# Kernel optimization log

Hardware: AMD Instinct MI355X
Metric: run time of the kernel (lower is better)

## Reference

```python
import jax, jax.numpy as jnp
import numpy as np

N_USER = 50000
N_ITEM = 100000
N = N_USER + N_ITEM
D = 64
NNZ = 2_400_000
B = 4096
N_LAYERS = 3
NEG_SLOPE = 0.01  # F.leaky_relu default
EPS = 1e-12       # F.normalize default eps


def setup_inputs() -> dict:
    key = jax.random.key(0)
    ks = jax.random.split(key, 12)
    s = 0.1  # xavier-ish scale
    return {
        "user_emb": jax.random.normal(ks[0], (N_USER, D), jnp.float32) * s,
        "item_emb": jax.random.normal(ks[1], (N_ITEM, D), jnp.float32) * s,
        "W_gc": jax.random.normal(ks[2], (N_LAYERS, D, D), jnp.float32) * s,
        "W_bi": jax.random.normal(ks[3], (N_LAYERS, D, D), jnp.float32) * s,
        "b_bi": jax.random.normal(ks[4], (N_LAYERS, 1, D), jnp.float32) * s,
        "vals": jax.random.uniform(ks[5], (NNZ,), jnp.float32) * (1.0 / 16.0),
        "rows": jax.random.randint(ks[6], (NNZ,), 0, N, jnp.int32),
        "cols": jax.random.randint(ks[7], (NNZ,), 0, N, jnp.int32),
        "users": jax.random.randint(ks[8], (B,), 0, N_USER, jnp.int32),
        "pos_items": jax.random.randint(ks[9], (B,), 0, N_ITEM, jnp.int32),
        "neg_items": jax.random.randint(ks[10], (B,), 0, N_ITEM, jnp.int32),
    }


def _spmm(rows, cols, vals, E, n):
    # sparse [n,n] (COO) @ dense [n,d]
    return jax.ops.segment_sum(vals[:, None] * E[cols], rows, num_segments=n)


def reference(user_emb, item_emb, W_gc, W_bi, b_bi, vals, rows, cols,
              users, pos_items, neg_items):
    n_user = user_emb.shape[0]
    n = n_user + item_emb.shape[0]
    ego = jnp.concatenate([user_emb, item_emb], axis=0)  # [N, D]
    all_embs = [ego]
    for k in range(N_LAYERS):
        L_side = _spmm(rows, cols, vals, ego, n)        # L @ E
        LI_side = L_side + ego                           # (L + I) @ E
        # NOTE: original code adds b_bi to BOTH branches (b_gc unused)
        sum_e = LI_side @ W_gc[k] + b_bi[k]
        bi_e = (L_side * ego) @ W_bi[k] + b_bi[k]
        ego = jax.nn.leaky_relu(sum_e + bi_e, NEG_SLOPE)
        norm = ego / jnp.maximum(
            jnp.linalg.norm(ego, axis=1, keepdims=True), EPS)
        all_embs.append(norm)
    all_embs = jnp.concatenate(all_embs, axis=1)         # [N, D*(L+1)]
    u_g = all_embs[:n_user][users]
    pos_g = all_embs[n_user:][pos_items]
    neg_g = all_embs[n_user:][neg_items]
    return (u_g, pos_g, neg_g)
```

## Files before the change

### kernel.cpp

```cpp
#include <hip/hip_runtime.h>

#define N_USER 50000
#define N_ITEM 100000
#define NTOT   150000
#define D      64
#define NNZ    2400000
#define NEG_SLOPE 0.01f

#define BSHIFT 10
#define NB     147
#define P1_PER 4096
#define NBLK1  586

typedef unsigned int uint;
typedef unsigned short ushort;
typedef _Float16 h4 __attribute__((ext_vector_type(4)));
typedef float f4 __attribute__((ext_vector_type(4)));

__device__ inline uint bf16rne(float x) {
    uint b = __float_as_uint(x);
    return (b + 0x7FFFu + ((b >> 16) & 1u)) >> 16;
}
__device__ inline float bf_lo(uint u) { return __uint_as_float(u << 16); }
__device__ inline float bf_hi(uint u) { return __uint_as_float(u & 0xFFFF0000u); }

__global__ void k_concat16(const float* __restrict__ u, const float* __restrict__ it,
                           ushort* __restrict__ A16) {
    int i = blockIdx.x * 256 + threadIdx.x;
    const int nu4 = N_USER * D / 4;
    float4 v = (i < nu4) ? ((const float4*)u)[i] : ((const float4*)it)[i - nu4];
    uint lo = bf16rne(v.x) | (bf16rne(v.y) << 16);
    uint hi = bf16rne(v.z) | (bf16rne(v.w) << 16);
    ((uint2*)A16)[i] = make_uint2(lo, hi);
}

__global__ void k_bzero(int* __restrict__ bcnt) {
    int t = threadIdx.x;
    if (t < NB) bcnt[t] = 0;
}

__global__ __launch_bounds__(1024) void k_bhist(const int* __restrict__ rows,
                                                int* __restrict__ bcnt) {
    __shared__ int lcnt[NB];
    int tid = threadIdx.x;
    if (tid < NB) lcnt[tid] = 0;
    __syncthreads();
    int base = blockIdx.x * P1_PER;
    #pragma unroll
    for (int k = 0; k < 4; ++k) {
        int i = base + k * 1024 + tid;
        if (i < NNZ) atomicAdd(&lcnt[rows[i] >> BSHIFT], 1);
    }
    __syncthreads();
    if (tid < NB) atomicAdd(&bcnt[tid], lcnt[tid]);
}

__global__ void k_bscan(const int* __restrict__ bcnt, int* __restrict__ bptr,
                        int* __restrict__ bcur) {
    __shared__ int s[256];
    int tid = threadIdx.x;
    int v = (tid < NB) ? bcnt[tid] : 0;
    s[tid] = v; __syncthreads();
    for (int off = 1; off < 256; off <<= 1) {
        int t = (tid >= off) ? s[tid - off] : 0;
        __syncthreads();
        s[tid] += t;
        __syncthreads();
    }
    if (tid < NB) { int ex = s[tid] - v; bptr[tid] = ex; bcur[tid] = ex; }
    if (tid == NB - 1) bptr[NB] = s[tid];
}

__global__ __launch_bounds__(1024) void k_binpass1(const int* __restrict__ rows,
                                                   const int* __restrict__ cols,
                                                   const float* __restrict__ vals,
                                                   int* __restrict__ bcur,
                                                   int2* __restrict__ bucketed) {
    __shared__ int lcnt[NB], lbase[NB];
    int tid = threadIdx.x;
    int base = blockIdx.x * P1_PER;
    if (tid < NB) lcnt[tid] = 0;
    __syncthreads();
    int r[4];
    #pragma unroll
    for (int k = 0; k < 4; ++k) {
        int i = base + k * 1024 + tid;
        r[k] = (i < NNZ) ? rows[i] : -1;
        if (r[k] >= 0) atomicAdd(&lcnt[r[k] >> BSHIFT], 1);
    }
    __syncthreads();
    if (tid < NB) { lbase[tid] = atomicAdd(&bcur[tid], lcnt[tid]); lcnt[tid] = 0; }
    __syncthreads();
    #pragma unroll
    for (int k = 0; k < 4; ++k) {
        int i = base + k * 1024 + tid;
        if (r[k] >= 0) {
            int b = r[k] >> BSHIFT;
            int off = atomicAdd(&lcnt[b], 1);
            bucketed[lbase[b] + off] =
                make_int2(((r[k] & 1023) << 18) | cols[i], __float_as_int(vals[i]));
        }
    }
}

__global__ __launch_bounds__(1024) void k_binpass2(const int* __restrict__ bptr,
                                                   const int2* __restrict__ bucketed,
                                                   int* __restrict__ ptr,
                                                   int2* __restrict__ csr) {
    __shared__ int c0[1024], px[1024];
    int tid = threadIdx.x, b = blockIdx.x;
    int s = bptr[b], e = bptr[b + 1];
    c0[tid] = 0;
    __syncthreads();
    for (int i = s + tid; i < e; i += 1024) atomicAdd(&c0[bucketed[i].x >> 18], 1);
    __syncthreads();
    int v = c0[tid];
    px[tid] = v;
    __syncthreads();
    for (int off = 1; off < 1024; off <<= 1) {
        int t = (tid >= off) ? px[tid - off] : 0;
        __syncthreads();
        px[tid] += t;
        __syncthreads();
    }
    int ex = px[tid] - v;
    int r = (b << BSHIFT) + tid;
    if (r <= NTOT) ptr[r] = s + ex;
    px[tid] = ex;
    c0[tid] = 0;
    __syncthreads();
    for (int i = s + tid; i < e; i += 1024) {
        int2 e2 = bucketed[i];
        int lr = e2.x >> 18;
        int off = atomicAdd(&c0[lr], 1);
        csr[s + px[lr] + off] = make_int2(e2.x & 0x3FFFF, e2.y);
    }
}

__global__ __launch_bounds__(256) void k_spmm(const int* __restrict__ ptr,
                                              const int2* __restrict__ csr,
                                              const ushort* __restrict__ E16,
                                              float* __restrict__ Lout) {
    int lane = threadIdx.x & 63;
    int half = lane >> 5;
    int l32  = lane & 31;
    int r = __builtin_amdgcn_readfirstlane(blockIdx.x * 4 + (threadIdx.x >> 6));
    int start = ptr[r], end = ptr[r + 1];
    float acc0 = 0.f, acc1 = 0.f;
    const uint* E32 = (const uint*)E16;
    int j = start;
    for (; j + 15 < end; j += 16) {
        int2 ea0 = csr[j + 0],  ea1 = csr[j + 1],  ea2 = csr[j + 2],  ea3 = csr[j + 3];
        int2 ea4 = csr[j + 4],  ea5 = csr[j + 5],  ea6 = csr[j + 6],  ea7 = csr[j + 7];
        int2 ea8 = csr[j + 8],  ea9 = csr[j + 9],  eaA = csr[j + 10], eaB = csr[j + 11];
        int2 eaC = csr[j + 12], eaD = csr[j + 13], eaE = csr[j + 14], eaF = csr[j + 15];
        int c0 = half ? ea1.x : ea0.x;
        int c1 = half ? ea3.x : ea2.x;
        int c2 = half ? ea5.x : ea4.x;
        int c3 = half ? ea7.x : ea6.x;
        int c4 = half ? ea9.x : ea8.x;
        int c5 = half ? eaB.x : eaA.x;
        int c6 = half ? eaD.x : eaC.x;
        int c7 = half ? eaF.x : eaE.x;
        uint u0 = E32[(c0 << 5) + l32];
        uint u1 = E32[(c1 << 5) + l32];
        uint u2 = E32[(c2 << 5) + l32];
        uint u3 = E32[(c3 << 5) + l32];
        uint u4 = E32[(c4 << 5) + l32];
        uint u5 = E32[(c5 << 5) + l32];
        uint u6 = E32[(c6 << 5) + l32];
        uint u7 = E32[(c7 << 5) + l32];
        float v0 = __int_as_float(half ? ea1.y : ea0.y);
        float v1 = __int_as_float(half ? ea3.y : ea2.y);
        float v2 = __int_as_float(half ? ea5.y : ea4.y);
        float v3 = __int_as_float(half ? ea7.y : ea6.y);
        float v4 = __int_as_float(half ? ea9.y : ea8.y);
        float v5 = __int_as_float(half ? eaB.y : eaA.y);
        float v6 = __int_as_float(half ? eaD.y : eaC.y);
        float v7 = __int_as_float(half ? eaF.y : eaE.y);
        acc0 += v0 * bf_lo(u0);  acc1 += v0 * bf_hi(u0);
        acc0 += v1 * bf_lo(u1);  acc1 += v1 * bf_hi(u1);
        acc0 += v2 * bf_lo(u2);  acc1 += v2 * bf_hi(u2);
        acc0 += v3 * bf_lo(u3);  acc1 += v3 * bf_hi(u3);
        acc0 += v4 * bf_lo(u4);  acc1 += v4 * bf_hi(u4);
        acc0 += v5 * bf_lo(u5);  acc1 += v5 * bf_hi(u5);
        acc0 += v6 * bf_lo(u6);  acc1 += v6 * bf_hi(u6);
        acc0 += v7 * bf_lo(u7);  acc1 += v7 * bf_hi(u7);
    }
    for (; j + 7 < end; j += 8) {
        int2 ea = csr[j + 0], eb = csr[j + 1];
        int2 ec = csr[j + 2], ed = csr[j + 3];
        int2 ee = csr[j + 4], ef = csr[j + 5];
        int2 eg = csr[j + 6], eh = csr[j + 7];
        int c0 = half ? eb.x : ea.x;
        int c1 = half ? ed.x : ec.x;
        int c2 = half ? ef.x : ee.x;
        int c3 = half ? eh.x : eg.x;
        uint u0 = E32[(c0 << 5) + l32];
        uint u1 = E32[(c1 << 5) + l32];
        uint u2 = E32[(c2 << 5) + l32];
        uint u3 = E32[(c3 << 5) + l32];
        float v0 = __int_as_float(half ? eb.y : ea.y);
        float v1 = __int_as_float(half ? ed.y : ec.y);
        float v2 = __int_as_float(half ? ef.y : ee.y);
        float v3 = __int_as_float(half ? eh.y : eg.y);
        acc0 += v0 * bf_lo(u0);  acc1 += v0 * bf_hi(u0);
        acc0 += v1 * bf_lo(u1);  acc1 += v1 * bf_hi(u1);
        acc0 += v2 * bf_lo(u2);  acc1 += v2 * bf_hi(u2);
        acc0 += v3 * bf_lo(u3);  acc1 += v3 * bf_hi(u3);
    }
    for (; j + 1 < end; j += 2) {
        int2 ea = csr[j], eb = csr[j + 1];
        int c   = half ? eb.x : ea.x;
        float v = __int_as_float(half ? eb.y : ea.y);
        uint u = E32[(c << 5) + l32];
        acc0 += v * bf_lo(u);  acc1 += v * bf_hi(u);
    }
    if (j < end) {
        int2 ea = csr[j];
        if (half == 0) {
            uint u = E32[(ea.x << 5) + l32];
            float v = __int_as_float(ea.y);
            acc0 += v * bf_lo(u);  acc1 += v * bf_hi(u);
        }
    }
    acc0 += __shfl_xor(acc0, 32, 64);
    acc1 += __shfl_xor(acc1, 32, 64);
    if (half == 0)
        *(float2*)&Lout[r * D + l32 * 2] = make_float2(acc0, acc1);
}

__global__ __launch_bounds__(256) void k_transform_mfma(
        const ushort* __restrict__ E16, const float* __restrict__ L,
        const float* __restrict__ Wgc, const float* __restrict__ Wbi,
        const float* __restrict__ bb, ushort* __restrict__ O16, int n) {
    __shared__ _Float16 ldsW[2 * 16 * 256];
    __shared__ ushort   ldsO[4][16 * 72];
    int tid = threadIdx.x;

    #pragma unroll
    for (int m = 0; m < 2; ++m) {
        const float* W = m ? Wbi : Wgc;
        for (int idx = tid; idx < 4096; idx += 256) {
            int k = idx >> 6, nn = idx & 63;
            ldsW[(m * 16 + (k >> 4) * 4 + (nn >> 4)) * 256 + (nn & 15) * 16 + (k & 15)] =
                (_Float16)W[idx];
        }
    }
    __syncthreads();

    int l = tid & 63, w = tid >> 6;
    int g = l >> 4, r16 = l & 15;

    h4 bfrag[2][4][4];
    #pragma unroll
    for (int m = 0; m < 2; ++m)
        #pragma unroll
        for (int ks = 0; ks < 4; ++ks)
            #pragma unroll
            for (int nt = 0; nt < 4; ++nt)
                bfrag[m][ks][nt] =
                    *(const h4*)&ldsW[(m * 16 + ks * 4 + nt) * 256 + r16 * 16 + g * 4];

    for (int t = 0; t < 4; ++t) {
        int tile = blockIdx.x * 4 + t;
        int rowbase = tile * 64 + w * 16;
        int r = rowbase + r16;
        int rc = min(r, n - 1);

        h4 x1[4], x2[4];
        #pragma unroll
        for (int ks = 0; ks < 4; ++ks) {
            int c = ks * 16 + g * 4;
            float4 lf = *(const float4*)&L[rc * D + c];
            uint2  eu = *(const uint2*)&E16[rc * D + c];
            float e0 = bf_lo(eu.x), e1 = bf_hi(eu.x);
            float e2 = bf_lo(eu.y), e3 = bf_hi(eu.y);
            x1[ks][0] = (_Float16)(lf.x + e0); x1[ks][1] = (_Float16)(lf.y + e1);
            x1[ks][2] = (_Float16)(lf.z + e2); x1[ks][3] = (_Float16)(lf.w + e3);
            x2[ks][0] = (_Float16)(lf.x * e0); x2[ks][1] = (_Float16)(lf.y * e1);
            x2[ks][2] = (_Float16)(lf.z * e2); x2[ks][3] = (_Float16)(lf.w * e3);
        }

        f4 acc[4];
        #pragma unroll
        for (int nt = 0; nt < 4; ++nt) acc[nt] = (f4){0.f, 0.f, 0.f, 0.f};
        #pragma unroll
        for (int ks = 0; ks < 4; ++ks)
            #pragma unroll
            for (int nt = 0; nt < 4; ++nt)
                acc[nt] = __builtin_amdgcn_mfma_f32_16x16x16f16(x1[ks], bfrag[0][ks][nt],
                                                                acc[nt], 0, 0, 0);
        #pragma unroll
        for (int ks = 0; ks < 4; ++ks)
            #pragma unroll
            for (int nt = 0; nt < 4; ++nt)
                acc[nt] = __builtin_amdgcn_mfma_f32_16x16x16f16(x2[ks], bfrag[1][ks][nt],
                                                                acc[nt], 0, 0, 0);

        #pragma unroll
        for (int nt = 0; nt < 4; ++nt) {
            int col = nt * 16 + r16;
            float bv = 2.f * bb[col];
            #pragma unroll
            for (int i = 0; i < 4; ++i) {
                float y = acc[nt][i] + bv;
                y = (y >= 0.f) ? y : NEG_SLOPE * y;
                ldsO[w][(g * 4 + i) * 72 + col] = (ushort)bf16rne(y);
            }
        }
        int lr = l >> 2;
        int rowg = rowbase + lr;
        if (rowg < n) {
            const ushort* src = &ldsO[w][lr * 72 + (l & 3) * 16];
            uint4 v0 = *(const uint4*)src;
            uint4 v1 = *(const uint4*)(src + 8);
            *(uint4*)&O16[rowg * D + (l & 3) * 16] = v0;
            *(uint4*)&O16[rowg * D + (l & 3) * 16 + 8] = v1;
        }
    }
}

__global__ void k_gather0(const float* __restrict__ u, const float* __restrict__ it,
                          const int* __restrict__ users, const int* __restrict__ pos,
                          const int* __restrict__ neg, float* __restrict__ out) {
    int lane = threadIdx.x & 63;
    int gi = blockIdx.x * 4 + (threadIdx.x >> 6);
    int g = gi >> 12, b = gi & 4095;
    const float* src = (g == 0) ? (u + (size_t)users[b] * D)
                                : (it + (size_t)((g == 1) ? pos[b] : neg[b]) * D);
    out[gi * 256 + lane] = src[lane];
}

__global__ void k_gathern(const ushort* __restrict__ E16, const int* __restrict__ users,
                          const int* __restrict__ pos, const int* __restrict__ neg,
                          float* __restrict__ out, int layer) {
    int lane = threadIdx.x & 63;
    int gi = blockIdx.x * 4 + (threadIdx.x >> 6);
    int g = gi >> 12, b = gi & 4095;
    int src = (g == 0) ? users[b] : (N_USER + ((g == 1) ? pos[b] : neg[b]));
    float v = __uint_as_float(((uint)E16[src * D + lane]) << 16);
    float ss = v * v;
    #pragma unroll
    for (int off = 32; off >= 1; off >>= 1) ss += __shfl_xor(ss, off, 64);
    float dnm = fmaxf(sqrtf(ss), 1e-12f);
    out[gi * 256 + layer * D + lane] = v / dnm;
}

extern "C" void kernel_launch(void* const* d_in, const int* in_sizes, int n_in,
                              void* d_out, int out_size, void* d_ws, size_t ws_size,
                              hipStream_t stream) {
    const float* user_emb = (const float*)d_in[0];
    const float* item_emb = (const float*)d_in[1];
    const float* W_gc     = (const float*)d_in[2];
    const float* W_bi     = (const float*)d_in[3];
    const float* b_bi     = (const float*)d_in[4];
    const float* vals     = (const float*)d_in[5];
    const int*   rows     = (const int*)d_in[6];
    const int*   cols     = (const int*)d_in[7];
    const int*   users    = (const int*)d_in[8];
    const int*   pos      = (const int*)d_in[9];
    const int*   neg      = (const int*)d_in[10];
    float* out = (float*)d_out;

    char* ws = (char*)d_ws;
    size_t off = 0;
    auto alloc = [&](size_t b) { void* p = ws + off; off += (b + 255) & ~(size_t)255; return p; };
    ushort* Ea  = (ushort*)alloc((size_t)NTOT * D * 2);
    ushort* Eb  = (ushort*)alloc((size_t)NTOT * D * 2);
    float*  L   = (float*) alloc((size_t)NTOT * D * 4);
    int2*   csr = (int2*)  alloc((size_t)NNZ * 8);
    int*    ptr = (int*)   alloc((size_t)(NTOT + 1) * 4);
    int*    bptr= (int*)   alloc((NB + 1) * 4);
    int*    bcnt= (int*)   alloc(NB * 4);
    int*    bcur= (int*)   alloc(NB * 4);
    int2*   bucketed = (int2*)L;
    (void)ws_size;

    hipLaunchKernelGGL(k_concat16, dim3(9375), dim3(256),  0, stream, user_emb, item_emb, Ea);
    hipLaunchKernelGGL(k_bzero,    dim3(1),    dim3(256),  0, stream, bcnt);
    hipLaunchKernelGGL(k_bhist,    dim3(NBLK1),dim3(1024), 0, stream, rows, bcnt);
    hipLaunchKernelGGL(k_bscan,    dim3(1),    dim3(256),  0, stream, bcnt, bptr, bcur);
    hipLaunchKernelGGL(k_binpass1, dim3(NBLK1),dim3(1024), 0, stream, rows, cols, vals, bcur, bucketed);
    hipLaunchKernelGGL(k_binpass2, dim3(NB),   dim3(1024), 0, stream, bptr, bucketed, ptr, csr);
    hipLaunchKernelGGL(k_gather0,  dim3(3072), dim3(256),  0, stream, user_emb, item_emb, users, pos, neg, out);

    ushort* cur = Ea; ushort* nxt = Eb;
    for (int k = 0; k < 3; ++k) {
        hipLaunchKernelGGL(k_spmm,           dim3(37500), dim3(256), 0, stream, ptr, csr, cur, L);
        hipLaunchKernelGGL(k_transform_mfma, dim3(586),   dim3(256), 0, stream, cur, L,
                           W_gc + k * 4096, W_bi + k * 4096, b_bi + k * 64, nxt, NTOT);
        hipLaunchKernelGGL(k_gathern,        dim3(3072),  dim3(256), 0, stream, nxt, users, pos, neg, out, k + 1);
        ushort* t = cur; cur = nxt; nxt = t;
    }
}
```

Baseline: 442.1 us.

## Fuse SpMM and MFMA transform into one per-layer kernel via LDS staging

Merges the sparse aggregation and the dense MFMA transform into a single kernel. Each wave computes 16 rows of L@E, forms the (L+E) and (L*E) operands in fp16 in LDS, and runs the MFMA directly. This removes the fp32 L intermediate write and re-read plus one launch per layer. In exchange each block repeats the weight staging, and each wave handles 16 rows serially, which lowers the parallelism available to hide gather latency. The bucketed scratch gets its own allocation.

```diff
diff --git a/kernel.cpp b/kernel.cpp
--- a/kernel.cpp
+++ b/kernel.cpp
@@ -11,6 +11,7 @@
 #define NB     147
 #define P1_PER 4096
 #define NBLK1  586
+#define NROWBLK 2344
 
 typedef unsigned int uint;
 typedef unsigned short ushort;
@@ -137,105 +138,14 @@
     }
 }
 
-__global__ __launch_bounds__(256) void k_spmm(const int* __restrict__ ptr,
-                                              const int2* __restrict__ csr,
-                                              const ushort* __restrict__ E16,
-                                              float* __restrict__ Lout) {
-    int lane = threadIdx.x & 63;
-    int half = lane >> 5;
-    int l32  = lane & 31;
-    int r = __builtin_amdgcn_readfirstlane(blockIdx.x * 4 + (threadIdx.x >> 6));
-    int start = ptr[r], end = ptr[r + 1];
-    float acc0 = 0.f, acc1 = 0.f;
-    const uint* E32 = (const uint*)E16;
-    int j = start;
-    for (; j + 15 < end; j += 16) {
-        int2 ea0 = csr[j + 0],  ea1 = csr[j + 1],  ea2 = csr[j + 2],  ea3 = csr[j + 3];
-        int2 ea4 = csr[j + 4],  ea5 = csr[j + 5],  ea6 = csr[j + 6],  ea7 = csr[j + 7];
-        int2 ea8 = csr[j + 8],  ea9 = csr[j + 9],  eaA = csr[j + 10], eaB = csr[j + 11];
-        int2 eaC = csr[j + 12], eaD = csr[j + 13], eaE = csr[j + 14], eaF = csr[j + 15];
-        int c0 = half ? ea1.x : ea0.x;
-        int c1 = half ? ea3.x : ea2.x;
-        int c2 = half ? ea5.x : ea4.x;
-        int c3 = half ? ea7.x : ea6.x;
-        int c4 = half ? ea9.x : ea8.x;
-        int c5 = half ? eaB.x : eaA.x;
-        int c6 = half ? eaD.x : eaC.x;
-        int c7 = half ? eaF.x : eaE.x;
-        uint u0 = E32[(c0 << 5) + l32];
-        uint u1 = E32[(c1 << 5) + l32];
-        uint u2 = E32[(c2 << 5) + l32];
-        uint u3 = E32[(c3 << 5) + l32];
-        uint u4 = E32[(c4 << 5) + l32];
-        uint u5 = E32[(c5 << 5) + l32];
-        uint u6 = E32[(c6 << 5) + l32];
-        uint u7 = E32[(c7 << 5) + l32];
-        float v0 = __int_as_float(half ? ea1.y : ea0.y);
-        float v1 = __int_as_float(half ? ea3.y : ea2.y);
-        float v2 = __int_as_float(half ? ea5.y : ea4.y);
-        float v3 = __int_as_float(half ? ea7.y : ea6.y);
-        float v4 = __int_as_float(half ? ea9.y : ea8.y);
-        float v5 = __int_as_float(half ? eaB.y : eaA.y);
-        float v6 = __int_as_float(half ? eaD.y : eaC.y);
-        float v7 = __int_as_float(half ? eaF.y : eaE.y);
-        acc0 += v0 * bf_lo(u0);  acc1 += v0 * bf_hi(u0);
-        acc0 += v1 * bf_lo(u1);  acc1 += v1 * bf_hi(u1);
-        acc0 += v2 * bf_lo(u2);  acc1 += v2 * bf_hi(u2);
-        acc0 += v3 * bf_lo(u3);  acc1 += v3 * bf_hi(u3);
-        acc0 += v4 * bf_lo(u4);  acc1 += v4 * bf_hi(u4);
-        acc0 += v5 * bf_lo(u5);  acc1 += v5 * bf_hi(u5);
-        acc0 += v6 * bf_lo(u6);  acc1 += v6 * bf_hi(u6);
-        acc0 += v7 * bf_lo(u7);  acc1 += v7 * bf_hi(u7);
-    }
-    for (; j + 7 < end; j += 8) {
-        int2 ea = csr[j + 0], eb = csr[j + 1];
-        int2 ec = csr[j + 2], ed = csr[j + 3];
-        int2 ee = csr[j + 4], ef = csr[j + 5];
-        int2 eg = csr[j + 6], eh = csr[j + 7];
-        int c0 = half ? eb.x : ea.x;
-        int c1 = half ? ed.x : ec.x;
-        int c2 = half ? ef.x : ee.x;
-        int c3 = half ? eh.x : eg.x;
-        uint u0 = E32[(c0 << 5) + l32];
-        uint u1 = E32[(c1 << 5) + l32];
-        uint u2 = E32[(c2 << 5) + l32];
-        uint u3 = E32[(c3 << 5) + l32];
-        float v0 = __int_as_float(half ? eb.y : ea.y);
-        float v1 = __int_as_float(half ? ed.y : ec.y);
-        float v2 = __int_as_float(half ? ef.y : ee.y);
-        float v3 = __int_as_float(half ? eh.y : eg.y);
-        acc0 += v0 * bf_lo(u0);  acc1 += v0 * bf_hi(u0);
-        acc0 += v1 * bf_lo(u1);  acc1 += v1 * bf_hi(u1);
-        acc0 += v2 * bf_lo(u2);  acc1 += v2 * bf_hi(u2);
-        acc0 += v3 * bf_lo(u3);  acc1 += v3 * bf_hi(u3);
-    }
-    for (; j + 1 < end; j += 2) {
-        int2 ea = csr[j], eb = csr[j + 1];
-        int c   = half ? eb.x : ea.x;
-        float v = __int_as_float(half ? eb.y : ea.y);
-        uint u = E32[(c << 5) + l32];
-        acc0 += v * bf_lo(u);  acc1 += v * bf_hi(u);
-    }
-    if (j < end) {
-        int2 ea = csr[j];
-        if (half == 0) {
-            uint u = E32[(ea.x << 5) + l32];
-            float v = __int_as_float(ea.y);
-            acc0 += v * bf_lo(u);  acc1 += v * bf_hi(u);
-        }
-    }
-    acc0 += __shfl_xor(acc0, 32, 64);
-    acc1 += __shfl_xor(acc1, 32, 64);
-    if (half == 0)
-        *(float2*)&Lout[r * D + l32 * 2] = make_float2(acc0, acc1);
-}
-
-__global__ __launch_bounds__(256) void k_transform_mfma(
-        const ushort* __restrict__ E16, const float* __restrict__ L,
+#define XPITCH 136
+__global__ __launch_bounds__(256) void k_layer(
+        const int* __restrict__ ptr, const int2* __restrict__ csr,
+        const ushort* __restrict__ E16,
         const float* __restrict__ Wgc, const float* __restrict__ Wbi,
-        const float* __restrict__ bb, ushort* __restrict__ O16, int n) {
+        const float* __restrict__ bb, ushort* __restrict__ O16) {
     __shared__ _Float16 ldsW[2 * 16 * 256];
-    __shared__ ushort   ldsO[4][16 * 72];
+    __shared__ ushort   xbuf[4][16 * XPITCH];
     int tid = threadIdx.x;
 
     #pragma unroll
@@ -249,8 +159,11 @@
     }
     __syncthreads();
 
-    int l = tid & 63, w = tid >> 6;
-    int g = l >> 4, r16 = l & 15;
+    int lane = tid & 63, w = tid >> 6;
+    int half = lane >> 5, l32 = lane & 31;
+    int g = lane >> 4, r16 = lane & 15;
+    const uint* E32 = (const uint*)E16;
+    _Float16* xw = (_Float16*)&xbuf[w][0];
 
     h4 bfrag[2][4][4];
     #pragma unroll
@@ -262,62 +175,142 @@
                 bfrag[m][ks][nt] =
                     *(const h4*)&ldsW[(m * 16 + ks * 4 + nt) * 256 + r16 * 16 + g * 4];
 
-    for (int t = 0; t < 4; ++t) {
-        int tile = blockIdx.x * 4 + t;
-        int rowbase = tile * 64 + w * 16;
-        int r = rowbase + r16;
-        int rc = min(r, n - 1);
-
-        h4 x1[4], x2[4];
+    int rowbase = blockIdx.x * 64 + w * 16;
+
+    for (int i = 0; i < 16; ++i) {
+        int r = rowbase + i;
+        int rr = __builtin_amdgcn_readfirstlane(min(r, NTOT - 1));
+        int start = ptr[rr], end = ptr[rr + 1];
+        float acc0 = 0.f, acc1 = 0.f;
+        int j = start;
+        for (; j + 15 < end; j += 16) {
+            int2 ea0 = csr[j + 0],  ea1 = csr[j + 1],  ea2 = csr[j + 2],  ea3 = csr[j + 3];
+            int2 ea4 = csr[j + 4],  ea5 = csr[j + 5],  ea6 = csr[j + 6],  ea7 = csr[j + 7];
+            int2 ea8 = csr[j + 8],  ea9 = csr[j + 9],  eaA = csr[j + 10], eaB = csr[j + 11];
+            int2 eaC = csr[j + 12], eaD = csr[j + 13], eaE = csr[j + 14], eaF = csr[j + 15];
+            int c0 = half ? ea1.x : ea0.x;
+            int c1 = half ? ea3.x : ea2.x;
+            int c2 = half ? ea5.x : ea4.x;
+            int c3 = half ? ea7.x : ea6.x;
+            int c4 = half ? ea9.x : ea8.x;
+            int c5 = half ? eaB.x : eaA.x;
+            int c6 = half ? eaD.x : eaC.x;
+            int c7 = half ? eaF.x : eaE.x;
+            uint u0 = E32[(c0 << 5) + l32];
+            uint u1 = E32[(c1 << 5) + l32];
+            uint u2 = E32[(c2 << 5) + l32];
+            uint u3 = E32[(c3 << 5) + l32];
+            uint u4 = E32[(c4 << 5) + l32];
+            uint u5 = E32[(c5 << 5) + l32];
+            uint u6 = E32[(c6 << 5) + l32];
+            uint u7 = E32[(c7 << 5) + l32];
+            float v0 = __int_as_float(half ? ea1.y : ea0.y);
+            float v1 = __int_as_float(half ? ea3.y : ea2.y);
+            float v2 = __int_as_float(half ? ea5.y : ea4.y);
+            float v3 = __int_as_float(half ? ea7.y : ea6.y);
+            float v4 = __int_as_float(half ? ea9.y : ea8.y);
+            float v5 = __int_as_float(half ? eaB.y : eaA.y);
+            float v6 = __int_as_float(half ? eaD.y : eaC.y);
+            float v7 = __int_as_float(half ? eaF.y : eaE.y);
+            acc0 += v0 * bf_lo(u0);  acc1 += v0 * bf_hi(u0);
+            acc0 += v1 * bf_lo(u1);  acc1 += v1 * bf_hi(u1);
+            acc0 += v2 * bf_lo(u2);  acc1 += v2 * bf_hi(u2);
+            acc0 += v3 * bf_lo(u3);  acc1 += v3 * bf_hi(u3);
+            acc0 += v4 * bf_lo(u4);  acc1 += v4 * bf_hi(u4);
+            acc0 += v5 * bf_lo(u5);  acc1 += v5 * bf_hi(u5);
+            acc0 += v6 * bf_lo(u6);  acc1 += v6 * bf_hi(u6);
+            acc0 += v7 * bf_lo(u7);  acc1 += v7 * bf_hi(u7);
+        }
+        for (; j + 7 < end; j += 8) {
+            int2 ea = csr[j + 0], eb = csr[j + 1];
+            int2 ec = csr[j + 2], ed = csr[j + 3];
+            int2 ee = csr[j + 4], ef = csr[j + 5];
+            int2 eg = csr[j + 6], eh = csr[j + 7];
+            int c0 = half ? eb.x : ea.x;
+            int c1 = half ? ed.x : ec.x;
+            int c2 = half ? ef.x : ee.x;
+            int c3 = half ? eh.x : eg.x;
+            uint u0 = E32[(c0 << 5) + l32];
+            uint u1 = E32[(c1 << 5) + l32];
+            uint u2 = E32[(c2 << 5) + l32];
+            uint u3 = E32[(c3 << 5) + l32];
+            float v0 = __int_as_float(half ? eb.y : ea.y);
+            float v1 = __int_as_float(half ? ed.y : ec.y);
+            float v2 = __int_as_float(half ? ef.y : ee.y);
+            float v3 = __int_as_float(half ? eh.y : eg.y);
+            acc0 += v0 * bf_lo(u0);  acc1 += v0 * bf_hi(u0);
+            acc0 += v1 * bf_lo(u1);  acc1 += v1 * bf_hi(u1);
+            acc0 += v2 * bf_lo(u2);  acc1 += v2 * bf_hi(u2);
+            acc0 += v3 * bf_lo(u3);  acc1 += v3 * bf_hi(u3);
+        }
+        for (; j + 1 < end; j += 2) {
+            int2 ea = csr[j], eb = csr[j + 1];
+            int c   = half ? eb.x : ea.x;
+            float v = __int_as_float(half ? eb.y : ea.y);
+            uint u = E32[(c << 5) + l32];
+            acc0 += v * bf_lo(u);  acc1 += v * bf_hi(u);
+        }
+        if (j < end) {
+            int2 ea = csr[j];
+            if (half == 0) {
+                uint u = E32[(ea.x << 5) + l32];
+                float v = __int_as_float(ea.y);
+                acc0 += v * bf_lo(u);  acc1 += v * bf_hi(u);
+            }
+        }
+        acc0 += __shfl_xor(acc0, 32, 64);
+        acc1 += __shfl_xor(acc1, 32, 64);
+
+        uint eu = E32[(rr << 5) + l32];
+        float e0 = bf_lo(eu), e1 = bf_hi(eu);
+        float p0 = half ? acc0 * e0 : acc0 + e0;
+        float p1 = half ? acc1 * e1 : acc1 + e1;
+        ushort2 pk;
+        pk.x = __builtin_bit_cast(ushort, (_Float16)p0);
+        pk.y = __builtin_bit_cast(ushort, (_Float16)p1);
+        *(ushort2*)&xw[i * XPITCH + half * 64 + 2 * l32] = pk;
+    }
+
+    f4 acc[4];
+    #pragma unroll
+    for (int nt = 0; nt < 4; ++nt) acc[nt] = (f4){0.f, 0.f, 0.f, 0.f};
+    #pragma unroll
+    for (int ks = 0; ks < 4; ++ks) {
+        h4 a1 = *(const h4*)&xw[r16 * XPITCH + ks * 16 + g * 4];
         #pragma unroll
-        for (int ks = 0; ks < 4; ++ks) {
-            int c = ks * 16 + g * 4;
-            float4 lf = *(const float4*)&L[rc * D + c];
-            uint2  eu = *(const uint2*)&E16[rc * D + c];
-            float e0 = bf_lo(eu.x), e1 = bf_hi(eu.x);
-            float e2 = bf_lo(eu.y), e3 = bf_hi(eu.y);
-            x1[ks][0] = (_Float16)(lf.x + e0); x1[ks][1] = (_Float16)(lf.y + e1);
-            x1[ks][2] = (_Float16)(lf.z + e2); x1[ks][3] = (_Float16)(lf.w + e3);
-            x2[ks][0] = (_Float16)(lf.x * e0); x2[ks][1] = (_Float16)(lf.y * e1);
-            x2[ks][2] = (_Float16)(lf.z * e2); x2[ks][3] = (_Float16)(lf.w * e3);
-        }
-
-        f4 acc[4];
+        for (int nt = 0; nt < 4; ++nt)
+            acc[nt] = __builtin_amdgcn_mfma_f32_16x16x16f16(a1, bfrag[0][ks][nt],
+                                                            acc[nt], 0, 0, 0);
+    }
+    #pragma unroll
+    for (int ks = 0; ks < 4; ++ks) {
+        h4 a2 = *(const h4*)&xw[r16 * XPITCH + 64 + ks * 16 + g * 4];
         #pragma unroll
-        for (int nt = 0; nt < 4; ++nt) acc[nt] = (f4){0.f, 0.f, 0.f, 0.f};
+        for (int nt = 0; nt < 4; ++nt)
+            acc[nt] = __builtin_amdgcn_mfma_f32_16x16x16f16(a2, bfrag[1][ks][nt],
+                                                            acc[nt], 0, 0, 0);
+    }
+
+    ushort* ow = &xbuf[w][0];
+    #pragma unroll
+    for (int nt = 0; nt < 4; ++nt) {
+        int col = nt * 16 + r16;
+        float bv = 2.f * bb[col];
         #pragma unroll
-        for (int ks = 0; ks < 4; ++ks)
-            #pragma unroll
-            for (int nt = 0; nt < 4; ++nt)
-                acc[nt] = __builtin_amdgcn_mfma_f32_16x16x16f16(x1[ks], bfrag[0][ks][nt],
-                                                                acc[nt], 0, 0, 0);
-        #pragma unroll
-        for (int ks = 0; ks < 4; ++ks)
-            #pragma unroll
-            for (int nt = 0; nt < 4; ++nt)
-                acc[nt] = __builtin_amdgcn_mfma_f32_16x16x16f16(x2[ks], bfrag[1][ks][nt],
-                                                                acc[nt], 0, 0, 0);
-
-        #pragma unroll
-        for (int nt = 0; nt < 4; ++nt) {
-            int col = nt * 16 + r16;
-            float bv = 2.f * bb[col];
-            #pragma unroll
-            for (int i = 0; i < 4; ++i) {
-                float y = acc[nt][i] + bv;
-                y = (y >= 0.f) ? y : NEG_SLOPE * y;
-                ldsO[w][(g * 4 + i) * 72 + col] = (ushort)bf16rne(y);
-            }
-        }
-        int lr = l >> 2;
-        int rowg = rowbase + lr;
-        if (rowg < n) {
-            const ushort* src = &ldsO[w][lr * 72 + (l & 3) * 16];
-            uint4 v0 = *(const uint4*)src;
-            uint4 v1 = *(const uint4*)(src + 8);
-            *(uint4*)&O16[rowg * D + (l & 3) * 16] = v0;
-            *(uint4*)&O16[rowg * D + (l & 3) * 16 + 8] = v1;
-        }
+        for (int i = 0; i < 4; ++i) {
+            float y = acc[nt][i] + bv;
+            y = (y >= 0.f) ? y : NEG_SLOPE * y;
+            ow[(g * 4 + i) * 72 + col] = (ushort)bf16rne(y);
+        }
+    }
+    int lr = lane >> 2;
+    int rowg = rowbase + lr;
+    if (rowg < NTOT) {
+        const ushort* src = &ow[lr * 72 + (lane & 3) * 16];
+        uint4 v0 = *(const uint4*)src;
+        uint4 v1 = *(const uint4*)(src + 8);
+        *(uint4*)&O16[rowg * D + (lane & 3) * 16] = v0;
+        *(uint4*)&O16[rowg * D + (lane & 3) * 16 + 8] = v1;
     }
 }
 
@@ -366,15 +359,14 @@
     char* ws = (char*)d_ws;
     size_t off = 0;
     auto alloc = [&](size_t b) { void* p = ws + off; off += (b + 255) & ~(size_t)255; return p; };
-    ushort* Ea  = (ushort*)alloc((size_t)NTOT * D * 2);
-    ushort* Eb  = (ushort*)alloc((size_t)NTOT * D * 2);
-    float*  L   = (float*) alloc((size_t)NTOT * D * 4);
-    int2*   csr = (int2*)  alloc((size_t)NNZ * 8);
-    int*    ptr = (int*)   alloc((size_t)(NTOT + 1) * 4);
-    int*    bptr= (int*)   alloc((NB + 1) * 4);
-    int*    bcnt= (int*)   alloc(NB * 4);
-    int*    bcur= (int*)   alloc(NB * 4);
-    int2*   bucketed = (int2*)L;
+    ushort* Ea   = (ushort*)alloc((size_t)NTOT * D * 2);
+    ushort* Eb   = (ushort*)alloc((size_t)NTOT * D * 2);
+    int2*   csr  = (int2*)  alloc((size_t)NNZ * 8);
+    int2*   bucketed = (int2*)alloc((size_t)NNZ * 8);
+    int*    ptr  = (int*)   alloc((size_t)(NTOT + 64) * 4);
+    int*    bptr = (int*)   alloc((NB + 1) * 4);
+    int*    bcnt = (int*)   alloc(NB * 4);
+    int*    bcur = (int*)   alloc(NB * 4);
     (void)ws_size;
 
     hipLaunchKernelGGL(k_concat16, dim3(9375), dim3(256),  0, stream, user_emb, item_emb, Ea);
@@ -387,10 +379,9 @@
 
     ushort* cur = Ea; ushort* nxt = Eb;
     for (int k = 0; k < 3; ++k) {
-        hipLaunchKernelGGL(k_spmm,           dim3(37500), dim3(256), 0, stream, ptr, csr, cur, L);
-        hipLaunchKernelGGL(k_transform_mfma, dim3(586),   dim3(256), 0, stream, cur, L,
-                           W_gc + k * 4096, W_bi + k * 4096, b_bi + k * 64, nxt, NTOT);
-        hipLaunchKernelGGL(k_gathern,        dim3(3072),  dim3(256), 0, stream, nxt, users, pos, neg, out, k + 1);
+        hipLaunchKernelGGL(k_layer,   dim3(NROWBLK), dim3(256), 0, stream, ptr, csr, cur,
+                           W_gc + k * 4096, W_bi + k * 4096, b_bi + k * 64, nxt);
+        hipLaunchKernelGGL(k_gathern, dim3(3072),    dim3(256), 0, stream, nxt, users, pos, neg, out, k + 1);
         ushort* t = cur; cur = nxt; nxt = t;
     }
 }
```

New measurement: 567.3 us. 1.28x slower.
